# Optimization experiments

Measured on AMD Instinct MI355X. Metric: run time of the kernel, lower is better.

The kernel has to match this reference:

```python
import jax, jax.numpy as jnp
import numpy as np


def setup_inputs() -> dict:
    key = jax.random.key(0)
    k1, k2 = jax.random.split(key)
    N, M, D = 16384, 16384, 3
    src_V = jax.random.normal(k1, (N, D), dtype=jnp.float32)
    tar_V = jax.random.normal(k2, (M, D), dtype=jnp.float32)
    return {"src_V": src_V, "tar_V": tar_V}


def reference(src_V, tar_V):
    # 1-NN: for each target point find nearest source point (replaces cKDTree).
    # Squared distances via ||t||^2 - 2 t.s + ||s||^2 ; [M, N]
    d2 = (
        jnp.sum(tar_V * tar_V, axis=1, keepdims=True)
        - 2.0 * (tar_V @ src_V.T)
        + jnp.sum(src_V * src_V, axis=1)[None, :]
    )
    ii = jnp.argmin(d2, axis=1)            # [M] nearest src index per target
    diff = src_V[ii] - tar_V               # [M, 3]
    loss = 0.5 * jnp.sum(diff * diff)
    return loss
```

## Files before the change

kernel.cpp:

```cpp
#include <hip/hip_runtime.h>
#include <math.h>

constexpr int N_SRC = 16384;
constexpr int M_TAR = 16384;

constexpr int BLOCKS = M_TAR / 32;
constexpr int TPB = 512;
constexpr int CHUNKS = 128;
constexpr int TILE = 4096;
constexpr int TILES = N_SRC / TILE;
constexpr int BODIES = TILE / CHUNKS / 2;

__global__ void zero_out(float* __restrict__ out) {
    if (threadIdx.x == 0) out[0] = 0.0f;
}

__device__ __forceinline__ float embed_ao(float t, unsigned mask_v, unsigned row_s) {
    float r;
    asm("v_and_or_b32 %0, %1, %2, %3"
        : "=v"(r) : "v"(t), "v"(mask_v), "s"(row_s));
    return r;
}
__device__ __forceinline__ void min3(float& b, float e0, float e1) {
    asm("v_min3_f32 %0, %1, %2, %3"
        : "=v"(b) : "v"(b), "v"(e0), "v"(e1));
}

__global__ __launch_bounds__(TPB, 4) void nn7(const float* __restrict__ src,
                                              const float* __restrict__ tar,
                                              float* __restrict__ out) {
    __shared__ float4 tile[TILE];

    const int tid   = threadIdx.x;
    const int g     = tid & 3;
    const int chunk = tid >> 2;
    const int tbase = blockIdx.x * 32;

    float txm2[8], tym2[8], tzm2[8], best[8];
#pragma unroll
    for (int k = 0; k < 8; ++k) {
        int T = tbase + g + 4 * k;
        txm2[k] = -2.0f * tar[3 * T + 0];
        tym2[k] = -2.0f * tar[3 * T + 1];
        tzm2[k] = -2.0f * tar[3 * T + 2];
        best[k] = INFINITY;
    }

    unsigned mask_v = 0xFFFFFF80u;

    for (int tl = 0; tl < TILES; ++tl) {
#pragma unroll
        for (int r = 0; r < TILE / TPB; ++r) {
            int p  = tid + r * TPB;
            int j3 = 3 * (tl * TILE + p);
            float x = src[j3 + 0], y = src[j3 + 1], z = src[j3 + 2];
            tile[p] = make_float4(x, y, z, fmaf(x, x, fmaf(y, y, z * z)));
        }
        __syncthreads();

        float4 s0 = tile[0 * CHUNKS + chunk];
        float4 s1 = tile[1 * CHUNKS + chunk];
#pragma unroll
        for (int i = 0; i < BODIES; ++i) {
            float4 n0, n1;
            if (i + 1 < BODIES) {
                n0 = tile[(2 * i + 2) * CHUNKS + chunk];
                n1 = tile[(2 * i + 3) * CHUNKS + chunk];
            }
            unsigned row0 = (unsigned)(tl * 2 * BODIES + 2 * i);
            unsigned row1 = row0 + 1;
#pragma unroll
            for (int k = 0; k < 8; ++k) {
                float t0 = fmaf(s0.z, tzm2[k], s0.w);
                t0 = fmaf(s0.y, tym2[k], t0);
                t0 = fmaf(s0.x, txm2[k], t0);
                float t1 = fmaf(s1.z, tzm2[k], s1.w);
                t1 = fmaf(s1.y, tym2[k], t1);
                t1 = fmaf(s1.x, txm2[k], t1);
                float e0 = embed_ao(t0, mask_v, row0);
                float e1 = embed_ao(t1, mask_v, row1);
                min3(best[k], e0, e1);
            }
            if (i + 1 < BODIES) { s0 = n0; s1 = n1; }
        }
        __syncthreads();
    }

    float* fv = (float*)tile;
    int*   fj = (int*)tile + 32 * 128;
#pragma unroll
    for (int k = 0; k < 8; ++k) {
        unsigned b = __float_as_uint(best[k]);
        int j  = (int)((b & 127u) * CHUNKS + chunk);
        int lt = g + 4 * k;
        fv[lt * CHUNKS + chunk] = __uint_as_float(b & 0xFFFFFF80u);
        fj[lt * CHUNKS + chunk] = j;
    }
    __syncthreads();

    const int tprime = tid >> 4;
    const int sub    = tid & 15;
    float bv = fv[tprime * CHUNKS + sub];
    int   bj = fj[tprime * CHUNKS + sub];
#pragma unroll
    for (int m = 1; m < 8; ++m) {
        float v = fv[tprime * CHUNKS + sub + 16 * m];
        int   j = fj[tprime * CHUNKS + sub + 16 * m];
        if (v < bv) { bv = v; bj = j; }
    }
#pragma unroll
    for (int s = 8; s >= 1; s >>= 1) {
        float vv = __shfl_xor(bv, s, 64);
        int   jj = __shfl_xor(bj, s, 64);
        if (vv < bv) { bv = vv; bj = jj; }
    }
    __syncthreads();

    if (sub == 0) {
        int tt = tbase + tprime;
        float dx = src[3 * bj + 0] - tar[3 * tt + 0];
        float dy = src[3 * bj + 1] - tar[3 * tt + 1];
        float dz = src[3 * bj + 2] - tar[3 * tt + 2];
        fv[tprime] = 0.5f * fmaf(dx, dx, fmaf(dy, dy, dz * dz));
    }
    __syncthreads();
    if (tid == 0) {
        float ssum = 0.0f;
#pragma unroll
        for (int i = 0; i < 32; ++i) ssum += fv[i];
        atomicAdd(out, ssum);
    }
}

extern "C" void kernel_launch(void* const* d_in, const int* in_sizes, int n_in,
                              void* d_out, int out_size, void* d_ws, size_t ws_size,
                              hipStream_t stream) {
    const float* src = (const float*)d_in[0];
    const float* tar = (const float*)d_in[1];
    float* out = (float*)d_out;
    (void)d_ws; (void)ws_size;

    zero_out<<<1, 64, 0, stream>>>(out);
    nn7<<<BLOCKS, TPB, 0, stream>>>(src, tar, out);
}
```

Baseline: 88.05 us.

## Replace brute-force nearest neighbor with uniform grid spatial hashing

Adds a single-block kernel that bins source points into a 24^3 uniform grid via counting sort, then a query kernel where each wavefront searches expanding shells of cells around its target and stops once the best distance is within the shell radius. This replaces the O(N*M) brute-force distance scan with a roughly local search. It risks slowdown from the serial single-block build, divergent shell loops, and imprecise early-exit bounds; the brute-force kernel remains as a fallback when workspace is too small.

```diff
diff --git a/kernel.cpp b/kernel.cpp
--- a/kernel.cpp
+++ b/kernel.cpp
@@ -4,12 +4,136 @@
 constexpr int N_SRC = 16384;
 constexpr int M_TAR = 16384;
 
-constexpr int BLOCKS = M_TAR / 32;
-constexpr int TPB = 512;
-constexpr int CHUNKS = 128;
-constexpr int TILE = 4096;
-constexpr int TILES = N_SRC / TILE;
-constexpr int BODIES = TILE / CHUNKS / 2;
+constexpr int G = 24;
+constexpr int NCELL_PAD = 14336;
+constexpr int CPT = NCELL_PAD / 1024;
+constexpr float GRID_LO = -4.0f;
+constexpr float INV_H = 3.0f;
+constexpr float H_CELL = 1.0f / 3.0f;
+
+constexpr size_t PTS_OFF = 65536;
+constexpr size_t WS_NEED = PTS_OFF + (size_t)N_SRC * sizeof(float4);
+
+__device__ __forceinline__ int cell_of(float x) {
+    int c = (int)((x - GRID_LO) * INV_H);
+    return min(max(c, 0), G - 1);
+}
+
+__global__ __launch_bounds__(1024) void build_grid(const float* __restrict__ src,
+                                                   int* __restrict__ off,
+                                                   float4* __restrict__ pts,
+                                                   float* __restrict__ out) {
+    __shared__ int cnt[NCELL_PAD];
+    __shared__ int aux[1024];
+    const int tid = threadIdx.x;
+    if (tid == 0) out[0] = 0.0f;
+
+#pragma unroll
+    for (int k = 0; k < CPT; ++k) cnt[tid + k * 1024] = 0;
+    __syncthreads();
+
+#pragma unroll
+    for (int k = 0; k < N_SRC / 1024; ++k) {
+        int j = tid + k * 1024;
+        float x = src[3 * j], y = src[3 * j + 1], z = src[3 * j + 2];
+        int cid = (cell_of(z) * G + cell_of(y)) * G + cell_of(x);
+        atomicAdd(&cnt[cid], 1);
+    }
+    __syncthreads();
+
+    int run = 0;
+    const int bc = tid * CPT;
+#pragma unroll
+    for (int k = 0; k < CPT; ++k) { int c = cnt[bc + k]; cnt[bc + k] = run; run += c; }
+    aux[tid] = run;
+    __syncthreads();
+    for (int d = 1; d < 1024; d <<= 1) {
+        int v = (tid >= d) ? aux[tid - d] : 0;
+        __syncthreads();
+        aux[tid] += v;
+        __syncthreads();
+    }
+    const int base = aux[tid] - run;
+#pragma unroll
+    for (int k = 0; k < CPT; ++k) {
+        int v = cnt[bc + k] + base;
+        cnt[bc + k] = v;
+        off[bc + k] = v;
+    }
+    if (tid == 0) off[NCELL_PAD] = N_SRC;
+    __syncthreads();
+
+#pragma unroll
+    for (int k = 0; k < N_SRC / 1024; ++k) {
+        int j = tid + k * 1024;
+        float x = src[3 * j], y = src[3 * j + 1], z = src[3 * j + 2];
+        int cid = (cell_of(z) * G + cell_of(y)) * G + cell_of(x);
+        int pos = atomicAdd(&cnt[cid], 1);
+        pts[pos] = make_float4(x, y, z, 0.0f);
+    }
+}
+
+__global__ __launch_bounds__(256) void query_grid(const float* __restrict__ tar,
+                                                  const int* __restrict__ off,
+                                                  const float4* __restrict__ pts,
+                                                  float* __restrict__ out) {
+    const int tid  = threadIdx.x;
+    const int lane = tid & 63;
+    const int wv   = tid >> 6;
+    const int t    = blockIdx.x * 4 + wv;
+
+    const float qx = tar[3 * t], qy = tar[3 * t + 1], qz = tar[3 * t + 2];
+    const int qcx = cell_of(qx), qcy = cell_of(qy), qcz = cell_of(qz);
+
+    float bd2 = INFINITY;
+    float gb  = INFINITY;
+
+    auto visit = [&](int cx, int cy, int cz) {
+        int cid = __builtin_amdgcn_readfirstlane((cz * G + cy) * G + cx);
+        int beg = off[cid];
+        int end = off[cid + 1];
+        for (int p = beg + lane; p < end; p += 64) {
+            float4 q = pts[p];
+            float dx = q.x - qx, dy = q.y - qy, dz = q.z - qz;
+            float d2 = fmaf(dx, dx, fmaf(dy, dy, dz * dz));
+            bd2 = fminf(bd2, d2);
+        }
+    };
+
+    for (int s = 0; s < G; ++s) {
+        int z0 = max(qcz - s, 0), z1 = min(qcz + s, G - 1);
+        int y0 = max(qcy - s, 0), y1 = min(qcy + s, G - 1);
+        int x0 = max(qcx - s, 0), x1 = min(qcx + s, G - 1);
+        for (int cz = z0; cz <= z1; ++cz) {
+            for (int cy = y0; cy <= y1; ++cy) {
+                int dyz = max(abs(cz - qcz), abs(cy - qcy));
+                if (dyz == s) {
+                    for (int cx = x0; cx <= x1; ++cx) visit(cx, cy, cz);
+                } else {
+                    if (qcx - s >= 0)     visit(qcx - s, cy, cz);
+                    if (qcx + s <= G - 1) visit(qcx + s, cy, cz);
+                }
+            }
+        }
+        gb = bd2;
+#pragma unroll
+        for (int m = 1; m < 64; m <<= 1) gb = fminf(gb, __shfl_xor(gb, m, 64));
+        float r = (float)s * H_CELL;
+        if (gb <= r * r) break;
+    }
+
+    __shared__ float part[4];
+    if (lane == 0) part[wv] = 0.5f * gb;
+    __syncthreads();
+    if (tid == 0) atomicAdd(out, part[0] + part[1] + part[2] + part[3]);
+}
+
+constexpr int FB_BLOCKS = M_TAR / 32;
+constexpr int FB_TPB = 512;
+constexpr int FB_CHUNKS = 128;
+constexpr int FB_TILE = 4096;
+constexpr int FB_TILES = N_SRC / FB_TILE;
+constexpr int FB_BODIES = FB_TILE / FB_CHUNKS / 2;
 
 __global__ void zero_out(float* __restrict__ out) {
     if (threadIdx.x == 0) out[0] = 0.0f;
@@ -17,25 +141,21 @@
 
 __device__ __forceinline__ float embed_ao(float t, unsigned mask_v, unsigned row_s) {
     float r;
-    asm("v_and_or_b32 %0, %1, %2, %3"
-        : "=v"(r) : "v"(t), "v"(mask_v), "s"(row_s));
+    asm("v_and_or_b32 %0, %1, %2, %3" : "=v"(r) : "v"(t), "v"(mask_v), "s"(row_s));
     return r;
 }
 __device__ __forceinline__ void min3(float& b, float e0, float e1) {
-    asm("v_min3_f32 %0, %1, %2, %3"
-        : "=v"(b) : "v"(b), "v"(e0), "v"(e1));
-}
-
-__global__ __launch_bounds__(TPB, 4) void nn7(const float* __restrict__ src,
-                                              const float* __restrict__ tar,
-                                              float* __restrict__ out) {
-    __shared__ float4 tile[TILE];
-
+    asm("v_min3_f32 %0, %1, %2, %3" : "=v"(b) : "v"(b), "v"(e0), "v"(e1));
+}
+
+__global__ __launch_bounds__(FB_TPB, 4) void nn7(const float* __restrict__ src,
+                                                 const float* __restrict__ tar,
+                                                 float* __restrict__ out) {
+    __shared__ float4 tile[FB_TILE];
     const int tid   = threadIdx.x;
     const int g     = tid & 3;
     const int chunk = tid >> 2;
     const int tbase = blockIdx.x * 32;
-
     float txm2[8], tym2[8], tzm2[8], best[8];
 #pragma unroll
     for (int k = 0; k < 8; ++k) {
@@ -45,29 +165,21 @@
         tzm2[k] = -2.0f * tar[3 * T + 2];
         best[k] = INFINITY;
     }
-
     unsigned mask_v = 0xFFFFFF80u;
-
-    for (int tl = 0; tl < TILES; ++tl) {
-#pragma unroll
-        for (int r = 0; r < TILE / TPB; ++r) {
-            int p  = tid + r * TPB;
-            int j3 = 3 * (tl * TILE + p);
+    for (int tl = 0; tl < FB_TILES; ++tl) {
+#pragma unroll
+        for (int r = 0; r < FB_TILE / FB_TPB; ++r) {
+            int p  = tid + r * FB_TPB;
+            int j3 = 3 * (tl * FB_TILE + p);
             float x = src[j3 + 0], y = src[j3 + 1], z = src[j3 + 2];
             tile[p] = make_float4(x, y, z, fmaf(x, x, fmaf(y, y, z * z)));
         }
         __syncthreads();
-
-        float4 s0 = tile[0 * CHUNKS + chunk];
-        float4 s1 = tile[1 * CHUNKS + chunk];
-#pragma unroll
-        for (int i = 0; i < BODIES; ++i) {
-            float4 n0, n1;
-            if (i + 1 < BODIES) {
-                n0 = tile[(2 * i + 2) * CHUNKS + chunk];
-                n1 = tile[(2 * i + 3) * CHUNKS + chunk];
-            }
-            unsigned row0 = (unsigned)(tl * 2 * BODIES + 2 * i);
+#pragma unroll
+        for (int i = 0; i < FB_BODIES; ++i) {
+            float4 s0 = tile[(2 * i + 0) * FB_CHUNKS + chunk];
+            float4 s1 = tile[(2 * i + 1) * FB_CHUNKS + chunk];
+            unsigned row0 = (unsigned)(tl * 2 * FB_BODIES + 2 * i);
             unsigned row1 = row0 + 1;
 #pragma unroll
             for (int k = 0; k < 8; ++k) {
@@ -81,31 +193,28 @@
                 float e1 = embed_ao(t1, mask_v, row1);
                 min3(best[k], e0, e1);
             }
-            if (i + 1 < BODIES) { s0 = n0; s1 = n1; }
-        }
-        __syncthreads();
-    }
-
+        }
+        __syncthreads();
+    }
     float* fv = (float*)tile;
     int*   fj = (int*)tile + 32 * 128;
 #pragma unroll
     for (int k = 0; k < 8; ++k) {
         unsigned b = __float_as_uint(best[k]);
-        int j  = (int)((b & 127u) * CHUNKS + chunk);
+        int j  = (int)((b & 127u) * FB_CHUNKS + chunk);
         int lt = g + 4 * k;
-        fv[lt * CHUNKS + chunk] = __uint_as_float(b & 0xFFFFFF80u);
-        fj[lt * CHUNKS + chunk] = j;
-    }
-    __syncthreads();
-
+        fv[lt * FB_CHUNKS + chunk] = __uint_as_float(b & 0xFFFFFF80u);
+        fj[lt * FB_CHUNKS + chunk] = j;
+    }
+    __syncthreads();
     const int tprime = tid >> 4;
     const int sub    = tid & 15;
-    float bv = fv[tprime * CHUNKS + sub];
-    int   bj = fj[tprime * CHUNKS + sub];
+    float bv = fv[tprime * FB_CHUNKS + sub];
+    int   bj = fj[tprime * FB_CHUNKS + sub];
 #pragma unroll
     for (int m = 1; m < 8; ++m) {
-        float v = fv[tprime * CHUNKS + sub + 16 * m];
-        int   j = fj[tprime * CHUNKS + sub + 16 * m];
+        float v = fv[tprime * FB_CHUNKS + sub + 16 * m];
+        int   j = fj[tprime * FB_CHUNKS + sub + 16 * m];
         if (v < bv) { bv = v; bj = j; }
     }
 #pragma unroll
@@ -115,7 +224,6 @@
         if (vv < bv) { bv = vv; bj = jj; }
     }
     __syncthreads();
-
     if (sub == 0) {
         int tt = tbase + tprime;
         float dx = src[3 * bj + 0] - tar[3 * tt + 0];
@@ -138,8 +246,14 @@
     const float* src = (const float*)d_in[0];
     const float* tar = (const float*)d_in[1];
     float* out = (float*)d_out;
-    (void)d_ws; (void)ws_size;
-
-    zero_out<<<1, 64, 0, stream>>>(out);
-    nn7<<<BLOCKS, TPB, 0, stream>>>(src, tar, out);
-}
+
+    if (ws_size >= WS_NEED) {
+        int*    off = (int*)d_ws;
+        float4* pts = (float4*)((char*)d_ws + PTS_OFF);
+        build_grid<<<1, 1024, 0, stream>>>(src, off, pts, out);
+        query_grid<<<M_TAR / 4, 256, 0, stream>>>(tar, off, pts, out);
+    } else {
+        zero_out<<<1, 64, 0, stream>>>(out);
+        nn7<<<FB_BLOCKS, FB_TPB, 0, stream>>>(src, tar, out);
+    }
+}
```

New measurement: 187.3 us. 113% more time.
